# Kernel tuning notes

Hardware: AMD Instinct MI355X
Metric: run time of the kernel (lower is better)

Reference implementation:

```python
import jax, jax.numpy as jnp
import numpy as np

N_NODES = 50000
N_EDGES = 300000
ANNOT = 200
HID = 256
N_STEPS = 8
N_BRANCH = 2


def setup_inputs() -> dict:
    key = jax.random.key(0)
    ks = jax.random.split(key, 12)
    s = 0.05
    return {
        "x": jax.random.normal(ks[0], (N_NODES, ANNOT), dtype=jnp.float32),
        "edge_index": jax.random.randint(ks[1], (2, N_EDGES), 0, N_NODES, dtype=jnp.int32),
        "batch": jnp.zeros((N_NODES,), dtype=jnp.int32),
        "W_reduce": jax.random.normal(ks[2], (HID, ANNOT), dtype=jnp.float32) * s,
        "b_reduce": jnp.zeros((HID,), dtype=jnp.float32),
        "W_ggc": jax.random.normal(ks[3], (N_STEPS, HID, HID), dtype=jnp.float32) * s,
        "W_ih": jax.random.normal(ks[4], (3 * HID, HID), dtype=jnp.float32) * s,
        "W_hh": jax.random.normal(ks[5], (3 * HID, HID), dtype=jnp.float32) * s,
        "b_ih": jnp.zeros((3 * HID,), dtype=jnp.float32),
        "b_hh": jnp.zeros((3 * HID,), dtype=jnp.float32),
        "W_lin": jax.random.normal(ks[6], (N_BRANCH, HID), dtype=jnp.float32) * s,
        "b_lin": jnp.zeros((N_BRANCH,), dtype=jnp.float32),
    }


def _gru_cell(m, h, W_ih, W_hh, b_ih, b_hh):
    # PyTorch GRUCell: gates ordered r, z, n
    gi = m @ W_ih.T + b_ih  # [N, 3H]
    gh = h @ W_hh.T + b_hh
    i_r, i_z, i_n = jnp.split(gi, 3, axis=1)
    h_r, h_z, h_n = jnp.split(gh, 3, axis=1)
    r = jax.nn.sigmoid(i_r + h_r)
    z = jax.nn.sigmoid(i_z + h_z)
    n = jnp.tanh(i_n + r * h_n)
    return (1.0 - z) * n + z * h


def reference(x, edge_index, batch, W_reduce, b_reduce, W_ggc, W_ih, W_hh, b_ih, b_hh, W_lin, b_lin):
    del batch  # unused by forward math
    n = x.shape[0]
    src, dst = edge_index[0], edge_index[1]

    h = x @ W_reduce.T + b_reduce  # [N, H]

    def step(h, Wi):
        m = h @ Wi                                    # per-step linear [N, H]
        agg = jax.ops.segment_sum(m[src], dst, num_segments=n)  # scatter-add to targets
        h_new = _gru_cell(agg, h, W_ih, W_hh, b_ih, b_hh)
        return h_new, None

    h, _ = jax.lax.scan(step, h, W_ggc)

    out = jax.nn.relu(h) @ W_lin.T + b_lin  # [N, 2]
    return jax.nn.log_softmax(out, axis=1)
```

## Files before the change

kernel.cpp:

```cpp
#include <hip/hip_runtime.h>

typedef _Float16 f16;
typedef unsigned short u16;
typedef unsigned int u32;
typedef _Float16 f16x4 __attribute__((ext_vector_type(4)));
typedef _Float16 f16x8 __attribute__((ext_vector_type(8)));
typedef float    floatx4 __attribute__((ext_vector_type(4)));

#define N_NODES 50000
#define N_EDGES 300000
#define ANNOT   200
#define KXP     224
#define HID     256

__device__ __forceinline__ floatx4 mfma_16x16x32_f16(f16x8 a, f16x8 b, floatx4 c) {
#if defined(__HIP_DEVICE_COMPILE__)
    return __builtin_amdgcn_mfma_f32_16x16x32_f16(a, b, c, 0, 0, 0);
#else
    return c;
#endif
}
__device__ __forceinline__ void gload_lds16(const f16* g, f16* l) {
#if defined(__HIP_DEVICE_COMPILE__)
    __builtin_amdgcn_global_load_lds((const __attribute__((address_space(1))) void*)g,
                                     (__attribute__((address_space(3))) void*)l, 16, 0, 0);
#else
    (void)g; (void)l;
#endif
}

__device__ __forceinline__ float sigm(float x) { return 1.0f / (1.0f + __expf(-x)); }
__device__ __forceinline__ float tanh_fast(float x) { return 1.0f - 2.0f / (1.0f + __expf(2.0f * x)); }

__device__ __forceinline__ float bf_bits_to_f32(u16 u) {
    union { u32 i; float f; } v; v.i = ((u32)u) << 16; return v.f;
}
__device__ __forceinline__ u16 f32_to_bf_bits(float f) {
    union { float f; u32 i; } v; v.f = f;
    u32 b = v.i;
    b += 0x7FFFu + ((b >> 16) & 1u);
    return (u16)(b >> 16);
}
__device__ __forceinline__ float load_in(const void* p, long i, int flag) {
    if (flag) return ((const float*)p)[i];
    return bf_bits_to_f32(((const u16*)p)[i]);
}

__global__ void probe_dtype(const u32* __restrict__ xw, int* __restrict__ flag) {
    __shared__ int cnt;
    if (threadIdx.x == 0) cnt = 0;
    __syncthreads();
    int c = 0;
    for (int i = threadIdx.x; i < 256; i += 64) {
        u32 lo = xw[i] & 0xFFFFu;
        u32 e = (lo >> 7) & 0xFFu;
        if (e >= 105u && e <= 140u) c++;
    }
    atomicAdd(&cnt, c);
    __syncthreads();
    if (threadIdx.x == 0) flag[0] = (cnt > 128) ? 0 : 1;
}

__global__ void cvt_f16(const void* __restrict__ in, f16* __restrict__ out, int n,
                        const int* __restrict__ flagp) {
    const int flag = *flagp;
    const int i = blockIdx.x * 256 + threadIdx.x;
    if (i < n) out[i] = (f16)load_in(in, i, flag);
}

__global__ void build_wrT(const void* __restrict__ Wre, f16* __restrict__ WrT,
                          const int* __restrict__ flagp) {
    const int flag = *flagp;
    const int i = blockIdx.x * 256 + threadIdx.x;
    if (i >= 256 * KXP) return;
    const int n = i / KXP, k = i - n * KXP;
    WrT[i] = (k < ANNOT) ? (f16)load_in(Wre, (long)n * ANNOT + k, flag) : (f16)0.0f;
}

__global__ void build_bb8(const f16* __restrict__ Wc, const void* __restrict__ Whh,
                          f16* __restrict__ Bb, const int* __restrict__ flagp) {
    const int flag = *flagp;
    const int i = blockIdx.x * 256 + threadIdx.x;
    const int s = i >> 19;
    const int rem = i & 524287;
    const int row = rem >> 9;
    const int k = rem & 511;
    const int chblk = row >> 7;
    const int r = row & 127;
    const int g = r >> 5;
    const int c = r & 31;
    const int ch = chblk * 32 + c;
    f16 v = (f16)0.0f;
    if (g == 0) {
        v = (k < 256) ? Wc[(long)ch * 2048 + s * 256 + k]
                      : (f16)load_in(Whh, (long)ch * 256 + (k - 256), flag);
    } else if (g == 1) {
        v = (k < 256) ? Wc[(long)(256 + ch) * 2048 + s * 256 + k]
                      : (f16)load_in(Whh, (long)(256 + ch) * 256 + (k - 256), flag);
    } else if (g == 2) {
        if (k < 256) v = Wc[(long)(512 + ch) * 2048 + s * 256 + k];
    } else {
        if (k >= 256) v = (f16)load_in(Whh, (long)(512 + ch) * 256 + (k - 256), flag);
    }
    Bb[i] = v;
}

__global__ void build_small(const void* b_ih, const void* b_hh, const void* b_red,
                            const void* W_lin, const void* b_lin,
                            float* __restrict__ sp, const int* __restrict__ flagp) {
    const int flag = *flagp;
    const int i = blockIdx.x * 256 + threadIdx.x;
    if (i < 512) {
        sp[i] = load_in(b_ih, i, flag) + load_in(b_hh, i, flag);
    } else if (i < 768) {
        sp[i] = load_in(b_ih, 512 + (i - 512), flag);
    } else if (i < 1024) {
        sp[i] = load_in(b_hh, 512 + (i - 768), flag);
    } else if (i < 1280) {
        sp[i] = load_in(b_red, i - 1024, flag);
    } else if (i < 1792) {
        sp[i] = load_in(W_lin, i - 1280, flag);
    } else if (i < 1794) {
        sp[i] = load_in(b_lin, i - 1792, flag);
    }
}

__global__ void build_xcvt(const void* __restrict__ x, f16* __restrict__ xc,
                           const int* __restrict__ flagp) {
    const int flag = *flagp;
    const long i = (long)blockIdx.x * 256 + threadIdx.x;
    if (i >= (long)N_NODES * KXP) return;
    const long r = i / KXP;
    const int  k = (int)(i - r * KXP);
    xc[i] = (k < ANNOT) ? (f16)load_in(x, r * ANNOT + k, flag) : (f16)0.0f;
}

__global__ void zero_i32(int* __restrict__ p, int n) {
    const int i = blockIdx.x * 256 + threadIdx.x;
    if (i < n) p[i] = 0;
}
__global__ void hist_kernel(const int* __restrict__ dst, int* __restrict__ deg, int n) {
    const int e = blockIdx.x * 256 + threadIdx.x;
    if (e < n) atomicAdd(&deg[dst[e]], 1);
}
__global__ void block_sum(const int* __restrict__ deg, int* __restrict__ partial, int n) {
    __shared__ int s[256];
    const int i = blockIdx.x * 256 + threadIdx.x;
    s[threadIdx.x] = (i < n) ? deg[i] : 0;
    __syncthreads();
    for (int off = 128; off > 0; off >>= 1) {
        if (threadIdx.x < off) s[threadIdx.x] += s[threadIdx.x + off];
        __syncthreads();
    }
    if (threadIdx.x == 0) partial[blockIdx.x] = s[0];
}
__global__ void scan_partials(int* __restrict__ partial, int nb, int* __restrict__ total_out) {
    __shared__ int s[256];
    const int t = threadIdx.x;
    s[t] = (t < nb) ? partial[t] : 0;
    __syncthreads();
    for (int off = 1; off < 256; off <<= 1) {
        int v = (t >= off) ? s[t - off] : 0;
        __syncthreads();
        s[t] += v;
        __syncthreads();
    }
    if (t < nb) partial[t] = (t == 0) ? 0 : s[t - 1];
    if (t == 0) *total_out = s[255];
}
__global__ void scan_block(const int* __restrict__ deg, const int* __restrict__ partial,
                           int* __restrict__ row_off, int* __restrict__ cursor, int n) {
    __shared__ int s[256];
    const int t = threadIdx.x;
    const int i = blockIdx.x * 256 + t;
    const int v = (i < n) ? deg[i] : 0;
    s[t] = v;
    __syncthreads();
    for (int off = 1; off < 256; off <<= 1) {
        int u = (t >= off) ? s[t - off] : 0;
        __syncthreads();
        s[t] += u;
        __syncthreads();
    }
    if (i < n) {
        const int v0 = partial[blockIdx.x] + s[t] - v;
        row_off[i] = v0;
        cursor[i]  = v0;
    }
}
__global__ void fill_kernel(const int* __restrict__ src, const int* __restrict__ dst,
                            int* __restrict__ cursor, int* __restrict__ csr, int n) {
    const int e = blockIdx.x * 256 + threadIdx.x;
    if (e < n) {
        const int p = atomicAdd(&cursor[dst[e]], 1);
        csr[p] = src[e];
    }
}

__global__ __launch_bounds__(256) void mgemm(
    const f16* __restrict__ A, int lda,
    const f16* __restrict__ Bt, int ldb,
    f16* __restrict__ C, int ldc,
    const float* __restrict__ bias,
    int M, int N, int K)
{
    __shared__ __attribute__((aligned(16))) f16 As[128 * 32];
    __shared__ __attribute__((aligned(16))) f16 Bs[128 * 32];
    const int tid  = threadIdx.x;
    const int lane = tid & 63;
    const int wave = tid >> 6;
    const int bm = blockIdx.x * 128;
    const int bn = blockIdx.y * 128;
    const int wm = (wave >> 1) * 64;
    const int wn = (wave & 1) * 64;
    const int quad = lane >> 4;
    const int l16  = lane & 15;

    floatx4 acc[4][4];
#pragma unroll
    for (int i = 0; i < 4; ++i)
#pragma unroll
        for (int j = 0; j < 4; ++j) acc[i][j] = (floatx4)(0.0f);

    for (int k0 = 0; k0 < K; k0 += 32) {
        __syncthreads();
#pragma unroll
        for (int it = 0; it < 2; ++it) {
            const int ci  = it * 256 + tid;
            const int row = ci >> 2;
            const int cg  = ci & 3;
            int ga = bm + row; if (ga > M - 1) ga = M - 1;
            gload_lds16(A + (long)ga * lda + k0 + cg * 8, As + ci * 8);
            gload_lds16(Bt + (long)(bn + row) * ldb + k0 + cg * 8, Bs + ci * 8);
        }
        __syncthreads();

        f16x8 af[4], bfv[4];
#pragma unroll
        for (int i = 0; i < 4; ++i) {
            af[i]  = *(const f16x8*)(As + (wm + i * 16 + l16) * 32 + quad * 8);
            bfv[i] = *(const f16x8*)(Bs + (wn + i * 16 + l16) * 32 + quad * 8);
        }
#pragma unroll
        for (int i = 0; i < 4; ++i)
#pragma unroll
            for (int j = 0; j < 4; ++j)
                acc[i][j] = mfma_16x16x32_f16(af[i], bfv[j], acc[i][j]);
    }

#pragma unroll
    for (int i = 0; i < 4; ++i) {
        const int r0 = bm + wm + i * 16 + quad * 4;
#pragma unroll
        for (int j = 0; j < 4; ++j) {
            const int col = bn + wn + j * 16 + l16;
            const float bv = bias ? bias[col] : 0.0f;
#pragma unroll
            for (int v = 0; v < 4; ++v) {
                const int r = r0 + v;
                if (r < M) C[(long)r * ldc + col] = (f16)(acc[i][j][v] + bv);
            }
        }
    }
}


#define GATES_STAGE(K0)                                                             \
    {                                                                               \
        __syncthreads();                                                            \
        _Pragma("unroll")                                                           \
        for (int it_ = 0; it_ < 4; ++it_) {                                         \
            const int ci_  = it_ * 256 + tid;                                       \
            const int row_ = ci_ >> 3;                                              \
            const int lc_  = (ci_ & 7) ^ (row_ & 7);                                \
            int ga_ = bm + row_; if (ga_ > M - 1) ga_ = M - 1;                      \
            gload_lds16(agh + (long)ga_ * 512 + (K0) + lc_ * 8, As + ci_ * 8);      \
            gload_lds16(Bb + (long)(cb * 128 + row_) * 512 + (K0) + lc_ * 8,        \
                        Bs + ci_ * 8);                                              \
        }                                                                           \
        __syncthreads();                                                            \
    }

#define GATES_STEP(KC, JJ)                                                          \
    {                                                                               \
        const int sl_ = (((KC) >> 3) + quad) ^ xr;                                  \
        f16x8 af_[4];                                                               \
        _Pragma("unroll")                                                           \
        for (int i_ = 0; i_ < 4; ++i_)                                              \
            af_[i_] = *(const f16x8*)(As + (wm + i_ * 16 + l16) * 64 + sl_ * 8);    \
        const f16x8 b0_ = *(const f16x8*)(Bs + (chh + l16) * 64 + sl_ * 8);         \
        const f16x8 b1_ = *(const f16x8*)(Bs + (32 + chh + l16) * 64 + sl_ * 8);    \
        const f16x8 b2_ = *(const f16x8*)(Bs + ((JJ) * 32 + chh + l16) * 64 + sl_ * 8); \
        _Pragma("unroll")                                                           \
        for (int i_ = 0; i_ < 4; ++i_) {                                            \
            acc[i_][0]    = mfma_16x16x32_f16(af_[i_], b0_, acc[i_][0]);            \
            acc[i_][1]    = mfma_16x16x32_f16(af_[i_], b1_, acc[i_][1]);            \
            acc[i_][(JJ)] = mfma_16x16x32_f16(af_[i_], b2_, acc[i_][(JJ)]);         \
        }                                                                           \
    }

__global__ __launch_bounds__(256) void gemm_gates(
    const f16* __restrict__ agh, const f16* __restrict__ Bb,
    f16* __restrict__ agh_nxt,
    const float* __restrict__ brz, const float* __restrict__ bin,
    const float* __restrict__ bhn, int M)
{
    const int lin = blockIdx.x;
    const int within = lin & 63;
    const int rb = (lin >> 6) * 8 + (within & 7);
    const int cb = within >> 3;
    if (rb * 128 >= M) return;

    __shared__ __attribute__((aligned(16))) f16 As[128 * 64];
    __shared__ __attribute__((aligned(16))) f16 Bs[128 * 64];
    const int tid  = threadIdx.x;
    const int lane = tid & 63;
    const int wave = tid >> 6;
    const int bm = rb * 128;
    const int wm  = (wave >> 1) * 64;
    const int chh = (wave & 1) * 16;
    const int quad = lane >> 4;
    const int l16  = lane & 15;
    const int xr   = l16 & 7;
    const int kcap0 = 256 + ((cb * 32) & ~63);
    const int koff  = (cb & 1) * 32;

    floatx4 acc[4][4];
#pragma unroll
    for (int i = 0; i < 4; ++i)
#pragma unroll
        for (int j = 0; j < 4; ++j) acc[i][j] = (floatx4)(0.0f);
    f16 h_frag[4][4] = {};

    for (int k0 = 0; k0 < 256; k0 += 64) {
        GATES_STAGE(k0)
        GATES_STEP(0, 2)
        GATES_STEP(32, 2)
    }
    for (int k0 = 256; k0 < 512; k0 += 64) {
        GATES_STAGE(k0)
        if (k0 == kcap0) {
#pragma unroll
            for (int i = 0; i < 4; ++i)
#pragma unroll
                for (int v = 0; v < 4; ++v) {
                    const int r = wm + i * 16 + quad * 4 + v;
                    const int kcol = koff + chh + l16;
                    const int slot = (kcol >> 3) ^ (r & 7);
                    h_frag[i][v] = As[r * 64 + slot * 8 + (kcol & 7)];
                }
        }
        GATES_STEP(0, 3)
        GATES_STEP(32, 3)
    }

    const int ch = cb * 32 + chh + l16;
    const float b_r  = brz[ch];
    const float b_z  = brz[256 + ch];
    const float b_in = bin[ch];
    const float b_hn = bhn[ch];
#pragma unroll
    for (int i = 0; i < 4; ++i) {
        const int r0 = bm + wm + i * 16 + quad * 4;
#pragma unroll
        for (int v = 0; v < 4; ++v) {
            const int r = r0 + v;
            if (r < M) {
                const float rg = sigm(acc[i][0][v] + b_r);
                const float zg = sigm(acc[i][1][v] + b_z);
                const float nn = tanh_fast(acc[i][2][v] + b_in + rg * (acc[i][3][v] + b_hn));
                const float ho = (float)h_frag[i][v];
                agh_nxt[(long)r * 512 + 256 + ch] = (f16)((1.0f - zg) * nn + zg * ho);
            }
        }
    }
}

__global__ __launch_bounds__(256) void aggregate(
    f16* __restrict__ agh, const int* __restrict__ row_off, const int* __restrict__ csr)
{
    const int node = blockIdx.x * 8 + (threadIdx.x >> 5);
    const int lane = threadIdx.x & 31;
    if (node >= N_NODES) return;
    const int e0 = row_off[node], e1 = row_off[node + 1];
    float a[8] = {0.0f, 0.0f, 0.0f, 0.0f, 0.0f, 0.0f, 0.0f, 0.0f};
    for (int e = e0; e < e1; ++e) {
        const int s = csr[e];
        const f16x8 v = *(const f16x8*)(agh + (long)s * 512 + 256 + lane * 8);
#pragma unroll
        for (int u = 0; u < 8; ++u) a[u] += (float)v[u];
    }
    f16x8 o;
#pragma unroll
    for (int u = 0; u < 8; ++u) o[u] = (f16)a[u];
    *(f16x8*)(agh + (long)node * 512 + lane * 8) = o;
}

__global__ __launch_bounds__(256) void final_kernel(
    const f16* __restrict__ h, const float* __restrict__ wlin,
    const float* __restrict__ blin, void* __restrict__ out,
    const int* __restrict__ flagp)
{
    const int flag = *flagp;
    const int node = blockIdx.x * 4 + (threadIdx.x >> 6);
    const int lane = threadIdx.x & 63;
    if (node >= N_NODES) return;
    const f16* hp = h + (long)node * 512;
    float a0 = 0.0f, a1 = 0.0f;
#pragma unroll
    for (int u = 0; u < 4; ++u) {
        const int c = lane * 4 + u;
        float hv = (float)hp[c];
        hv = hv > 0.0f ? hv : 0.0f;
        a0 += hv * wlin[c];
        a1 += hv * wlin[256 + c];
    }
#pragma unroll
    for (int off = 32; off > 0; off >>= 1) {
        a0 += __shfl_down(a0, off);
        a1 += __shfl_down(a1, off);
    }
    if (lane == 0) {
        a0 += blin[0];
        a1 += blin[1];
        const float mx  = fmaxf(a0, a1);
        const float lse = mx + logf(expf(a0 - mx) + expf(a1 - mx));
        const float o0 = a0 - lse, o1 = a1 - lse;
        if (flag) {
            ((float*)out)[(long)node * 2]     = o0;
            ((float*)out)[(long)node * 2 + 1] = o1;
        } else {
            ((u16*)out)[(long)node * 2]     = f32_to_bf_bits(o0);
            ((u16*)out)[(long)node * 2 + 1] = f32_to_bf_bits(o1);
        }
    }
}

extern "C" void kernel_launch(void* const* d_in, const int* in_sizes, int n_in,
                              void* d_out, int out_size, void* d_ws, size_t ws_size,
                              hipStream_t stream)
{
    (void)in_sizes; (void)n_in; (void)out_size; (void)ws_size;
    const void* x        = d_in[0];
    const int*  ei       = (const int*)d_in[1];
    const void* W_reduce = d_in[3];
    const void* b_reduce = d_in[4];
    const void* W_ggc    = d_in[5];
    const void* W_ih     = d_in[6];
    const void* W_hh     = d_in[7];
    const void* b_ih     = d_in[8];
    const void* b_hh     = d_in[9];
    const void* W_lin    = d_in[10];
    const void* b_lin    = d_in[11];
    const int* src = ei;
    const int* dst = ei + N_EDGES;

    char* w = (char*)d_ws;
    auto carve = [&](size_t bytes) -> char* {
        char* p = w;
        w += (bytes + 255) & ~(size_t)255;
        return p;
    };
    f16* agh_a = (f16*)carve((size_t)N_NODES * 512 * 2);
    f16* agh_b = (f16*)carve((size_t)N_NODES * 512 * 2);
    f16* x_cvt = agh_b;
    f16*   WrT   = (f16*)carve((size_t)256 * KXP * 2);
    f16*   Wih16 = (f16*)carve((size_t)768 * 256 * 2);
    f16*   Wg16  = (f16*)carve((size_t)2048 * 256 * 2);
    f16*   Wc    = (f16*)carve((size_t)768 * 2048 * 2);
    f16*   Bb8   = (f16*)carve((size_t)8 * 1024 * 512 * 2);
    float* sp    = (float*)carve(2048 * 4);
    int*   flag  = (int*)carve(256);
    int* deg     = (int*)carve((size_t)N_NODES * 4);
    int* row_off = (int*)carve((size_t)(N_NODES + 1) * 4);
    int* cursor  = (int*)carve((size_t)N_NODES * 4);
    int* csr     = (int*)carve((size_t)N_EDGES * 4);
    int* partial = (int*)carve(256 * 4);

    float* brz  = sp;
    float* bin  = sp + 512;
    float* bhn  = sp + 768;
    float* br0  = sp + 1024;
    float* wlin = sp + 1280;
    float* blin = sp + 1792;

    probe_dtype<<<1, 64, 0, stream>>>((const u32*)x, flag);

    cvt_f16<<<(768 * 256 + 255) / 256, 256, 0, stream>>>(W_ih, Wih16, 768 * 256, flag);
    cvt_f16<<<(2048 * 256 + 255) / 256, 256, 0, stream>>>(W_ggc, Wg16, 2048 * 256, flag);
    build_wrT<<<(256 * KXP + 255) / 256, 256, 0, stream>>>(W_reduce, WrT, flag);
    build_small<<<8, 256, 0, stream>>>(b_ih, b_hh, b_reduce, W_lin, b_lin, sp, flag);
    build_xcvt<<<(int)(((long)N_NODES * KXP + 255) / 256), 256, 0, stream>>>(x, x_cvt, flag);

    zero_i32<<<196, 256, 0, stream>>>(deg, N_NODES);
    hist_kernel<<<(N_EDGES + 255) / 256, 256, 0, stream>>>(dst, deg, N_EDGES);
    block_sum<<<196, 256, 0, stream>>>(deg, partial, N_NODES);
    scan_partials<<<1, 256, 0, stream>>>(partial, 196, row_off + N_NODES);
    scan_block<<<196, 256, 0, stream>>>(deg, partial, row_off, cursor, N_NODES);
    fill_kernel<<<(N_EDGES + 255) / 256, 256, 0, stream>>>(src, dst, cursor, csr, N_EDGES);

    mgemm<<<dim3(6, 16), 256, 0, stream>>>(Wih16, 256, Wg16, 256, Wc, 2048,
                                           (const float*)nullptr, 768, 2048, 256);
    build_bb8<<<(8 * 1024 * 512) / 256, 256, 0, stream>>>(Wc, W_hh, Bb8, flag);

    mgemm<<<dim3(391, 2), 256, 0, stream>>>(x_cvt, KXP, WrT, KXP, agh_a + 256, 512, br0,
                                            N_NODES, 256, KXP);

    for (int s = 0; s < 8; ++s) {
        f16* cur = (s & 1) ? agh_b : agh_a;
        f16* nxt = (s & 1) ? agh_a : agh_b;
        aggregate<<<6250, 256, 0, stream>>>(cur, row_off, csr);
        gemm_gates<<<49 * 64, 256, 0, stream>>>(cur, Bb8 + (size_t)s * 524288, nxt,
                                                brz, bin, bhn, N_NODES);
    }

    final_kernel<<<12500, 256, 0, stream>>>(agh_a + 256, wlin, blin, d_out, flag);
}
```

Baseline: 1.157 ms.

## Widen gates GEMM tile to 64 channels per block and unroll aggregation by two

The fused GRU-gates GEMM now computes 64 hidden channels per block instead of 32. It loads a 192-row B tile so each A tile staged in LDS feeds twice as many MFMAs, and the grid shrinks from 49*64 to 49*32 blocks. This cuts redundant global/LDS traffic for the activation operand, at the cost of doubled accumulator registers (4x2x4 floatx4) and more LDS, which may lower occupancy. Separately, the CSR aggregation loop handles two edges per iteration with two accumulators to expose more memory-level parallelism. The early-exit check on out-of-range row blocks was removed; its safety depends on row clamping and the r<M guard.

```diff
diff --git a/kernel.cpp b/kernel.cpp
--- a/kernel.cpp
+++ b/kernel.cpp
@@ -265,7 +265,7 @@
 }
 
 
-#define GATES_STAGE(K0)                                                             \
+#define GATES_STAGE2(K0, GHI)                                                       \
     {                                                                               \
         __syncthreads();                                                            \
         _Pragma("unroll")                                                           \
@@ -275,27 +275,42 @@
             const int lc_  = (ci_ & 7) ^ (row_ & 7);                                \
             int ga_ = bm + row_; if (ga_ > M - 1) ga_ = M - 1;                      \
             gload_lds16(agh + (long)ga_ * 512 + (K0) + lc_ * 8, As + ci_ * 8);      \
-            gload_lds16(Bb + (long)(cb * 128 + row_) * 512 + (K0) + lc_ * 8,        \
-                        Bs + ci_ * 8);                                              \
+        }                                                                           \
+        _Pragma("unroll")                                                           \
+        for (int it_ = 0; it_ < 6; ++it_) {                                         \
+            const int ci_  = it_ * 256 + tid;                                       \
+            const int lr_  = ci_ >> 3;                                              \
+            const int lc_  = (ci_ & 7) ^ (lr_ & 7);                                 \
+            const int chl_ = (lr_ >= 96) ? 1 : 0;                                   \
+            const int rem_ = lr_ - chl_ * 96;                                       \
+            const int g_   = rem_ >> 5;                                             \
+            const int c_   = rem_ & 31;                                             \
+            const int gm_  = (g_ == 2 && (GHI)) ? 3 : g_;                           \
+            const int grow_ = cbp * 256 + chl_ * 128 + gm_ * 32 + c_;               \
+            gload_lds16(Bb + (long)grow_ * 512 + (K0) + lc_ * 8, Bs + ci_ * 8);     \
         }                                                                           \
         __syncthreads();                                                            \
     }
 
-#define GATES_STEP(KC, JJ)                                                          \
+#define GATES_STEP2(KC, GS2)                                                        \
     {                                                                               \
         const int sl_ = (((KC) >> 3) + quad) ^ xr;                                  \
         f16x8 af_[4];                                                               \
         _Pragma("unroll")                                                           \
         for (int i_ = 0; i_ < 4; ++i_)                                              \
             af_[i_] = *(const f16x8*)(As + (wm + i_ * 16 + l16) * 64 + sl_ * 8);    \
-        const f16x8 b0_ = *(const f16x8*)(Bs + (chh + l16) * 64 + sl_ * 8);         \
-        const f16x8 b1_ = *(const f16x8*)(Bs + (32 + chh + l16) * 64 + sl_ * 8);    \
-        const f16x8 b2_ = *(const f16x8*)(Bs + ((JJ) * 32 + chh + l16) * 64 + sl_ * 8); \
         _Pragma("unroll")                                                           \
-        for (int i_ = 0; i_ < 4; ++i_) {                                            \
-            acc[i_][0]    = mfma_16x16x32_f16(af_[i_], b0_, acc[i_][0]);            \
-            acc[i_][1]    = mfma_16x16x32_f16(af_[i_], b1_, acc[i_][1]);            \
-            acc[i_][(JJ)] = mfma_16x16x32_f16(af_[i_], b2_, acc[i_][(JJ)]);         \
+        for (int c2_ = 0; c2_ < 2; ++c2_) {                                         \
+            const int rbase_ = jc * 96 + c2_ * 16 + l16;                            \
+            const f16x8 b0_ = *(const f16x8*)(Bs + (long)(rbase_) * 64 + sl_ * 8);  \
+            const f16x8 b1_ = *(const f16x8*)(Bs + (long)(rbase_ + 32) * 64 + sl_ * 8); \
+            const f16x8 b2_ = *(const f16x8*)(Bs + (long)(rbase_ + 64) * 64 + sl_ * 8); \
+            _Pragma("unroll")                                                       \
+            for (int i_ = 0; i_ < 4; ++i_) {                                        \
+                acc[i_][c2_][0]     = mfma_16x16x32_f16(af_[i_], b0_, acc[i_][c2_][0]);     \
+                acc[i_][c2_][1]     = mfma_16x16x32_f16(af_[i_], b1_, acc[i_][c2_][1]);     \
+                acc[i_][c2_][(GS2)] = mfma_16x16x32_f16(af_[i_], b2_, acc[i_][c2_][(GS2)]); \
+            }                                                                       \
         }                                                                           \
     }
 
@@ -306,71 +321,77 @@
     const float* __restrict__ bhn, int M)
 {
     const int lin = blockIdx.x;
-    const int within = lin & 63;
-    const int rb = (lin >> 6) * 8 + (within & 7);
-    const int cb = within >> 3;
-    if (rb * 128 >= M) return;
+    const int within = lin & 31;
+    const int rb = (lin >> 5) * 8 + (within & 7);
+    const int cbp = within >> 3;
 
     __shared__ __attribute__((aligned(16))) f16 As[128 * 64];
-    __shared__ __attribute__((aligned(16))) f16 Bs[128 * 64];
+    __shared__ __attribute__((aligned(16))) f16 Bs[192 * 64];
     const int tid  = threadIdx.x;
     const int lane = tid & 63;
     const int wave = tid >> 6;
     const int bm = rb * 128;
     const int wm  = (wave >> 1) * 64;
-    const int chh = (wave & 1) * 16;
+    const int jc  = wave & 1;
     const int quad = lane >> 4;
     const int l16  = lane & 15;
     const int xr   = l16 & 7;
-    const int kcap0 = 256 + ((cb * 32) & ~63);
-    const int koff  = (cb & 1) * 32;
-
-    floatx4 acc[4][4];
+    const int kcap = 256 + cbp * 64;
+
+    floatx4 acc[4][2][4];
 #pragma unroll
     for (int i = 0; i < 4; ++i)
 #pragma unroll
-        for (int j = 0; j < 4; ++j) acc[i][j] = (floatx4)(0.0f);
-    f16 h_frag[4][4] = {};
+        for (int c2 = 0; c2 < 2; ++c2)
+#pragma unroll
+            for (int g = 0; g < 4; ++g) acc[i][c2][g] = (floatx4)(0.0f);
+    f16 h_frag[4][2][4] = {};
 
     for (int k0 = 0; k0 < 256; k0 += 64) {
-        GATES_STAGE(k0)
-        GATES_STEP(0, 2)
-        GATES_STEP(32, 2)
+        GATES_STAGE2(k0, 0)
+        GATES_STEP2(0, 2)
+        GATES_STEP2(32, 2)
     }
     for (int k0 = 256; k0 < 512; k0 += 64) {
-        GATES_STAGE(k0)
-        if (k0 == kcap0) {
+        GATES_STAGE2(k0, 1)
+        if (k0 == kcap) {
 #pragma unroll
             for (int i = 0; i < 4; ++i)
 #pragma unroll
-                for (int v = 0; v < 4; ++v) {
-                    const int r = wm + i * 16 + quad * 4 + v;
-                    const int kcol = koff + chh + l16;
-                    const int slot = (kcol >> 3) ^ (r & 7);
-                    h_frag[i][v] = As[r * 64 + slot * 8 + (kcol & 7)];
+                for (int c2 = 0; c2 < 2; ++c2)
+#pragma unroll
+                    for (int v = 0; v < 4; ++v) {
+                        const int r = wm + i * 16 + quad * 4 + v;
+                        const int kcol = jc * 32 + c2 * 16 + l16;
+                        const int slot = (kcol >> 3) ^ (r & 7);
+                        h_frag[i][c2][v] = As[r * 64 + slot * 8 + (kcol & 7)];
+                    }
+        }
+        GATES_STEP2(0, 3)
+        GATES_STEP2(32, 3)
+    }
+
+#pragma unroll
+    for (int c2 = 0; c2 < 2; ++c2) {
+        const int ch = cbp * 64 + jc * 32 + c2 * 16 + l16;
+        const float b_r  = brz[ch];
+        const float b_z  = brz[256 + ch];
+        const float b_in = bin[ch];
+        const float b_hn = bhn[ch];
+#pragma unroll
+        for (int i = 0; i < 4; ++i) {
+            const int r0 = bm + wm + i * 16 + quad * 4;
+#pragma unroll
+            for (int v = 0; v < 4; ++v) {
+                const int r = r0 + v;
+                if (r < M) {
+                    const float rg = sigm(acc[i][c2][0][v] + b_r);
+                    const float zg = sigm(acc[i][c2][1][v] + b_z);
+                    const float nn = tanh_fast(acc[i][c2][2][v] + b_in +
+                                               rg * (acc[i][c2][3][v] + b_hn));
+                    const float ho = (float)h_frag[i][c2][v];
+                    agh_nxt[(long)r * 512 + 256 + ch] = (f16)((1.0f - zg) * nn + zg * ho);
                 }
-        }
-        GATES_STEP(0, 3)
-        GATES_STEP(32, 3)
-    }
-
-    const int ch = cb * 32 + chh + l16;
-    const float b_r  = brz[ch];
-    const float b_z  = brz[256 + ch];
-    const float b_in = bin[ch];
-    const float b_hn = bhn[ch];
-#pragma unroll
-    for (int i = 0; i < 4; ++i) {
-        const int r0 = bm + wm + i * 16 + quad * 4;
-#pragma unroll
-        for (int v = 0; v < 4; ++v) {
-            const int r = r0 + v;
-            if (r < M) {
-                const float rg = sigm(acc[i][0][v] + b_r);
-                const float zg = sigm(acc[i][1][v] + b_z);
-                const float nn = tanh_fast(acc[i][2][v] + b_in + rg * (acc[i][3][v] + b_hn));
-                const float ho = (float)h_frag[i][v];
-                agh_nxt[(long)r * 512 + 256 + ch] = (f16)((1.0f - zg) * nn + zg * ho);
             }
         }
     }
@@ -384,15 +405,25 @@
     if (node >= N_NODES) return;
     const int e0 = row_off[node], e1 = row_off[node + 1];
     float a[8] = {0.0f, 0.0f, 0.0f, 0.0f, 0.0f, 0.0f, 0.0f, 0.0f};
-    for (int e = e0; e < e1; ++e) {
-        const int s = csr[e];
-        const f16x8 v = *(const f16x8*)(agh + (long)s * 512 + 256 + lane * 8);
-#pragma unroll
-        for (int u = 0; u < 8; ++u) a[u] += (float)v[u];
+    float b[8] = {0.0f, 0.0f, 0.0f, 0.0f, 0.0f, 0.0f, 0.0f, 0.0f};
+    int e = e0;
+    for (; e + 2 <= e1; e += 2) {
+        const int s0 = csr[e];
+        const int s1 = csr[e + 1];
+        const f16x8 v0 = *(const f16x8*)(agh + (long)s0 * 512 + 256 + lane * 8);
+        const f16x8 v1 = *(const f16x8*)(agh + (long)s1 * 512 + 256 + lane * 8);
+#pragma unroll
+        for (int u = 0; u < 8; ++u) { a[u] += (float)v0[u]; b[u] += (float)v1[u]; }
+    }
+    if (e < e1) {
+        const int s0 = csr[e];
+        const f16x8 v0 = *(const f16x8*)(agh + (long)s0 * 512 + 256 + lane * 8);
+#pragma unroll
+        for (int u = 0; u < 8; ++u) a[u] += (float)v0[u];
     }
     f16x8 o;
 #pragma unroll
-    for (int u = 0; u < 8; ++u) o[u] = (f16)a[u];
+    for (int u = 0; u < 8; ++u) o[u] = (f16)(a[u] + b[u]);
     *(f16x8*)(agh + (long)node * 512 + lane * 8) = o;
 }
 
@@ -510,7 +541,7 @@
         f16* cur = (s & 1) ? agh_b : agh_a;
         f16* nxt = (s & 1) ? agh_a : agh_b;
         aggregate<<<6250, 256, 0, stream>>>(cur, row_off, csr);
-        gemm_gates<<<49 * 64, 256, 0, stream>>>(cur, Bb8 + (size_t)s * 524288, nxt,
+        gemm_gates<<<49 * 32, 256, 0, stream>>>(cur, Bb8 + (size_t)s * 524288, nxt,
                                                 brz, bin, bhn, N_NODES);
     }
 
```

New measurement: 1.355 ms. 17.1% more time.
